# Kernel optimization log

Hardware: AMD Instinct MI355X
Metric: run time of the kernel (lower is better)

## Reference

```python
import jax, jax.numpy as jnp
import numpy as np
import math

B, LQ, LK = 4, 512, 512
D_MODEL, NHEAD, NLABELS = 512, 8, 8
D_Q = D_MODEL // NHEAD


def setup_inputs() -> dict:
    key = jax.random.key(0)
    ks = jax.random.split(key, 12)
    xavier = lambda k, shape: jax.random.uniform(
        k, shape, jnp.float32,
        -math.sqrt(6.0 / (shape[0] + shape[1])), math.sqrt(6.0 / (shape[0] + shape[1])))
    return {
        "q": jax.random.normal(ks[0], (B, LQ, D_MODEL), jnp.float32),
        "k": jax.random.normal(ks[1], (B, LK, D_MODEL), jnp.float32),
        "edge_mask": jax.random.randint(ks[2], (B, LQ, LK, NLABELS), 0, 2).astype(jnp.float32),
        "padding_mask": jax.random.randint(ks[3], (B, LQ, LK), 0, 2).astype(jnp.float32),
        "w_q_w": xavier(ks[4], (D_MODEL, D_MODEL)),
        "w_q_b": jnp.zeros((D_MODEL,), jnp.float32),
        "w_k": xavier(ks[5], (D_MODEL, D_MODEL)),
        "w_v": xavier(ks[6], (D_MODEL, D_MODEL)),
        "w_h_w": xavier(ks[7], (D_MODEL, D_MODEL)),
        "w_h_b": jnp.zeros((D_MODEL,), jnp.float32),
        "b_ks": xavier(ks[8], (NLABELS, D_Q)),
        "b_vs": xavier(ks[9], (NLABELS, D_Q)),
    }


def reference(q, k, edge_mask, padding_mask, w_q_w, w_q_b, w_k, w_v, w_h_w, w_h_b, b_ks, b_vs):
    sz_b, len_q, _ = q.shape
    len_k = k.shape[1]
    temp = np.power(D_Q, 0.5).astype(np.float32)

    # projections -> (nhead, B, L, d_q), matching torch permute(2,0,1,3)
    query = (q @ w_q_w.T + w_q_b).reshape(sz_b, len_q, NHEAD, D_Q).transpose(2, 0, 1, 3)
    key = (k @ w_k.T).reshape(sz_b, len_k, NHEAD, D_Q).transpose(2, 0, 1, 3)
    value = (k @ w_v.T).reshape(sz_b, len_k, NHEAD, D_Q).transpose(2, 0, 1, 3)

    # content scores + relation-bias scores
    qk = jnp.einsum('hbqd,hbkd->hbqk', query, key)
    key_rel = jnp.einsum('bqkl,ld->bqkd', edge_mask, b_ks)      # (B,Lq,Lk,d_q)
    qkr = jnp.einsum('hbqd,bqkd->hbqk', query, key_rel)
    output_attention_weights = (qk + qkr) / temp                # pre-mask, as returned by torch

    # mask where no edge label AND padding_mask==1
    relation_mask = (edge_mask.sum(-1) + (1.0 - padding_mask)) == 0  # (B,Lq,Lk)
    rm = relation_mask[None, :, :, :]                                # broadcast over heads
    attn = jnp.where(rm, -jnp.inf, output_attention_weights)
    attn = jax.nn.softmax(attn, axis=-1)
    attn = jnp.where(rm, 0.0, attn)

    # value aggregation: content + relation values
    qv = jnp.einsum('hbqk,hbkd->hbqd', attn, value)
    val_rel = jnp.einsum('bqkl,ld->bqkd', edge_mask, b_vs)
    qvr = jnp.einsum('hbqk,bqkd->hbqd', attn, val_rel)

    out = (qv + qvr).transpose(1, 2, 0, 3).reshape(sz_b, len_q, D_MODEL)
    out = out @ w_h_w.T + w_h_b
    return out, output_attention_weights.reshape(NHEAD * sz_b, len_q, len_k)
```

## Files before the change

kernel.cpp:

```cpp
#include <hip/hip_runtime.h>
#include <math.h>

#define NB 4
#define LQ 512
#define LK 512
#define DM 512
#define NH 8
#define DQ 64
#define NL 8

typedef short bf16x8 __attribute__((ext_vector_type(8)));
typedef float f32x4 __attribute__((ext_vector_type(4)));

__device__ __forceinline__ unsigned short f2bf(float x) {
    unsigned u = __float_as_uint(x);
    u += 0x7fff + ((u >> 16) & 1);
    return (unsigned short)(u >> 16);
}
__device__ __forceinline__ float bf2f(unsigned x) {
    return __uint_as_float(x << 16);
}

__device__ __forceinline__ void gld16(const void* g, void* l) {
    __builtin_amdgcn_global_load_lds(
        (const __attribute__((address_space(1))) void*)g,
        (__attribute__((address_space(3))) void*)l, 16, 0, 0);
}

template<int BM, int BN, int WR, int WC, int MI, int NI>
__device__ __forceinline__ void mfma_core(const unsigned short* __restrict__ Ag, int lda,
                                          const unsigned short* __restrict__ Bg, int ldb,
                                          int K, short* As, short* Bs,
                                          f32x4 (&acc)[MI][NI]) {
    const int tid = threadIdx.x;
    const int wave = tid >> 6, lane = tid & 63;
    const int quad = lane >> 4, l16 = lane & 15;
    const int wr = wave / WC, wc = wave % WC;
    constexpr int WMT = BM / WR, WNT = BN / WC;

    for (int k0 = 0; k0 < K; k0 += 32) {
        __syncthreads();
#pragma unroll
        for (int s = 0; s < BM / 64; ++s) {
            const int c = s * 256 + tid;
            gld16(Ag + (size_t)(c >> 2) * lda + k0 + (c & 3) * 8,
                  (char*)As + s * 4096 + wave * 1024);
        }
#pragma unroll
        for (int s = 0; s < BN / 64; ++s) {
            const int c = s * 256 + tid;
            gld16(Bg + (size_t)(c >> 2) * ldb + k0 + (c & 3) * 8,
                  (char*)Bs + s * 4096 + wave * 1024);
        }
        __syncthreads();

        bf16x8 af[MI], bf[NI];
#pragma unroll
        for (int i = 0; i < MI; ++i)
            af[i] = *(const bf16x8*)&As[(wr * WMT + i * 16 + l16) * 32 + quad * 8];
#pragma unroll
        for (int j = 0; j < NI; ++j)
            bf[j] = *(const bf16x8*)&Bs[(wc * WNT + j * 16 + l16) * 32 + quad * 8];
#pragma unroll
        for (int i = 0; i < MI; ++i)
#pragma unroll
            for (int j = 0; j < NI; ++j)
                acc[i][j] = __builtin_amdgcn_mfma_f32_16x16x32_bf16(af[i], bf[j], acc[i][j], 0, 0, 0);
    }
}

__global__ __launch_bounds__(256) void convert_kernel(
        const float* __restrict__ s0, const float* __restrict__ s1,
        const float* __restrict__ s2, const float* __restrict__ s3,
        const float* __restrict__ s4, const float* __restrict__ s5,
        unsigned short* __restrict__ d0, unsigned short* __restrict__ d1,
        unsigned short* __restrict__ d2, unsigned short* __restrict__ d3,
        unsigned short* __restrict__ d4, unsigned short* __restrict__ d5) {
    const float* s; unsigned short* d; int n;
    switch (blockIdx.y) {
        case 0: s = s0; d = d0; n = NB * LQ * DM; break;
        case 1: s = s1; d = d1; n = NB * LK * DM; break;
        case 2: s = s2; d = d2; n = DM * DM; break;
        case 3: s = s3; d = d3; n = DM * DM; break;
        case 4: s = s4; d = d4; n = DM * DM; break;
        default: s = s5; d = d5; n = DM * DM; break;
    }
    const int i = blockIdx.x * 256 + threadIdx.x;
    if (i * 8 >= n) return;
    const float4* sv = (const float4*)s;
    const float4 a = sv[2 * (size_t)i], b = sv[2 * (size_t)i + 1];
    uint4 o;
    o.x = (unsigned)f2bf(a.x) | ((unsigned)f2bf(a.y) << 16);
    o.y = (unsigned)f2bf(a.z) | ((unsigned)f2bf(a.w) << 16);
    o.z = (unsigned)f2bf(b.x) | ((unsigned)f2bf(b.y) << 16);
    o.w = (unsigned)f2bf(b.z) | ((unsigned)f2bf(b.w) << 16);
    *(uint4*)(d + (size_t)i * 8) = o;
}

__global__ __launch_bounds__(256) void proj_all(const unsigned short* __restrict__ qbf,
                                                const unsigned short* __restrict__ kbf,
                                                const unsigned short* __restrict__ wqb,
                                                const unsigned short* __restrict__ wkb,
                                                const unsigned short* __restrict__ wvb,
                                                const float* __restrict__ w_q_b,
                                                unsigned short* __restrict__ Qp,
                                                unsigned short* __restrict__ Kp,
                                                unsigned short* __restrict__ Vt) {
    __shared__ __align__(16) short As[64 * 32];
    __shared__ __align__(16) short Bs[64 * 32];
    const unsigned short* A; const unsigned short* W; const float* bias;
    unsigned short* C; int mode;
    switch (blockIdx.z) {
        case 0:  A = qbf; W = wqb; bias = w_q_b; C = Qp; mode = 0; break;
        case 1:  A = kbf; W = wkb; bias = nullptr; C = Kp; mode = 0; break;
        default: A = kbf; W = wvb; bias = nullptr; C = Vt; mode = 1; break;
    }
    f32x4 acc[2][2];
    const f32x4 zz = {0.f, 0.f, 0.f, 0.f};
#pragma unroll
    for (int i = 0; i < 2; ++i)
#pragma unroll
        for (int j = 0; j < 2; ++j) acc[i][j] = zz;
    const int m0 = blockIdx.x * 64, n0 = blockIdx.y * 64;
    mfma_core<64, 64, 2, 2, 2, 2>(A + (size_t)m0 * DM, DM, W + (size_t)n0 * DM, DM, DM, As, Bs, acc);
    const int tid = threadIdx.x, wave = tid >> 6, lane = tid & 63;
    const int quad = lane >> 4, l16 = lane & 15;
    const int wr = wave >> 1, wc = wave & 1;
#pragma unroll
    for (int i = 0; i < 2; ++i)
#pragma unroll
        for (int r = 0; r < 4; ++r) {
            const int gm = m0 + wr * 32 + i * 16 + quad * 4 + r;
#pragma unroll
            for (int j = 0; j < 2; ++j) {
                const int gn = n0 + wc * 32 + j * 16 + l16;
                float v = acc[i][j][r];
                if (bias) v += bias[gn];
                if (mode == 0) C[(size_t)gm * DM + gn] = f2bf(v);
                else C[(size_t)(gm >> 9) * (DM * LK) + (size_t)gn * LK + (gm & 511)] = f2bf(v);
            }
        }
}

__global__ __launch_bounds__(256) void qk_mfma(const unsigned short* __restrict__ Qp,
                                               const unsigned short* __restrict__ Kp,
                                               unsigned short* __restrict__ Sc) {
    __shared__ __align__(16) short As[64 * 32];
    __shared__ __align__(16) short Bs[64 * 32];
    f32x4 acc[2][2];
    const f32x4 zz = {0.f, 0.f, 0.f, 0.f};
#pragma unroll
    for (int i = 0; i < 2; ++i)
#pragma unroll
        for (int j = 0; j < 2; ++j) acc[i][j] = zz;
    const int z = blockIdx.z, h = z >> 2, b = z & 3;
    const int m0 = blockIdx.x * 64, n0 = blockIdx.y * 64;
    const unsigned short* Ag = Qp + (size_t)(b * LQ + m0) * DM + h * DQ;
    const unsigned short* Bg = Kp + (size_t)(b * LK + n0) * DM + h * DQ;
    mfma_core<64, 64, 2, 2, 2, 2>(Ag, DM, Bg, DM, DQ, As, Bs, acc);
    const int tid = threadIdx.x, wave = tid >> 6, lane = tid & 63;
    const int quad = lane >> 4, l16 = lane & 15;
    const int wr = wave >> 1, wc = wave & 1;
    unsigned short* Cz = Sc + (size_t)z * LQ * LK;
#pragma unroll
    for (int i = 0; i < 2; ++i)
#pragma unroll
        for (int r = 0; r < 4; ++r) {
            const int gm = m0 + wr * 32 + i * 16 + quad * 4 + r;
#pragma unroll
            for (int j = 0; j < 2; ++j) {
                const int gn = n0 + wc * 32 + j * 16 + l16;
                Cz[(size_t)gm * LK + gn] = f2bf(acc[i][j][r]);
            }
        }
}

__global__ __launch_bounds__(512) void softmax_kernel(const float* __restrict__ em,
                                                      const float* __restrict__ pad,
                                                      const unsigned short* __restrict__ Qp,
                                                      const float* __restrict__ b_ks,
                                                      const unsigned short* __restrict__ Sc,
                                                      float* __restrict__ weights,
                                                      unsigned short* __restrict__ attn,
                                                      float* __restrict__ Tb) {
    const int tid = threadIdx.x, wave = tid >> 6, lane = tid & 63;
    const int bq = blockIdx.x, b = bq >> 9, q = bq & 511;
    const int h = wave, z = h * NB + b;

    const float qd = bf2f(Qp[(size_t)bq * DM + h * DQ + lane]);
    float sv[NL];
#pragma unroll
    for (int l = 0; l < NL; ++l) {
        float p = qd * b_ks[l * DQ + lane];
#pragma unroll
        for (int o = 1; o < 64; o <<= 1) p += __shfl_xor(p, o, 64);
        sv[l] = p;
    }

    float4 ev[16];
    const float* eb = em + (size_t)bq * (LK * NL);
#pragma unroll
    for (int j = 0; j < 8; ++j) {
        const int k = lane + 64 * j;
        ev[2 * j]     = *(const float4*)(eb + k * 8);
        ev[2 * j + 1] = *(const float4*)(eb + k * 8 + 4);
    }
    float padv[8];
#pragma unroll
    for (int j = 0; j < 8; ++j) padv[j] = pad[(size_t)bq * LK + lane + 64 * j];
    const unsigned short* sp = Sc + ((size_t)z * LQ + q) * LK;
    float qk8[8];
#pragma unroll
    for (int j = 0; j < 8; ++j) qk8[j] = bf2f(sp[lane + 64 * j]);

    const size_t rowbase = ((size_t)z * LQ + q) * LK;
    float wv8[8], m8[8];
#pragma unroll
    for (int j = 0; j < 8; ++j) {
        const float4 a = ev[2 * j], c = ev[2 * j + 1];
        const float rel = a.x * sv[0] + a.y * sv[1] + a.z * sv[2] + a.w * sv[3]
                        + c.x * sv[4] + c.y * sv[5] + c.z * sv[6] + c.w * sv[7];
        const float es = ((a.x + a.y) + (a.z + a.w)) + ((c.x + c.y) + (c.z + c.w));
        const float wv = (qk8[j] + rel) * 0.125f;
        wv8[j] = wv;
        m8[j] = ((es + 1.0f - padv[j]) == 0.0f) ? -__builtin_inff() : wv;
        weights[rowbase + lane + 64 * j] = wv;
    }

    float mx = m8[0];
#pragma unroll
    for (int j = 1; j < 8; ++j) mx = fmaxf(mx, m8[j]);
#pragma unroll
    for (int o = 1; o < 64; o <<= 1) mx = fmaxf(mx, __shfl_xor(mx, o, 64));

    float e8[8], ss = 0.f;
#pragma unroll
    for (int j = 0; j < 8; ++j) { e8[j] = __expf(m8[j] - mx); ss += e8[j]; }
#pragma unroll
    for (int o = 1; o < 64; o <<= 1) ss += __shfl_xor(ss, o, 64);
    const float inv = 1.0f / ss;

    float tl[NL] = {0.f, 0.f, 0.f, 0.f, 0.f, 0.f, 0.f, 0.f};
#pragma unroll
    for (int j = 0; j < 8; ++j) {
        const float a_ = e8[j] * inv;
        attn[rowbase + lane + 64 * j] = f2bf(a_);
        const float4 a = ev[2 * j], c = ev[2 * j + 1];
        tl[0] = fmaf(a_, a.x, tl[0]); tl[1] = fmaf(a_, a.y, tl[1]);
        tl[2] = fmaf(a_, a.z, tl[2]); tl[3] = fmaf(a_, a.w, tl[3]);
        tl[4] = fmaf(a_, c.x, tl[4]); tl[5] = fmaf(a_, c.y, tl[5]);
        tl[6] = fmaf(a_, c.z, tl[6]); tl[7] = fmaf(a_, c.w, tl[7]);
    }
#pragma unroll
    for (int o = 1; o < 64; o <<= 1)
#pragma unroll
        for (int l = 0; l < NL; ++l) tl[l] += __shfl_xor(tl[l], o, 64);
    if (lane == 0) {
        float* tp = Tb + ((size_t)z * LQ + q) * NL;
#pragma unroll
        for (int l = 0; l < NL; ++l) tp[l] = tl[l];
    }
}

__global__ __launch_bounds__(256) void qv_mfma(const unsigned short* __restrict__ Attn,
                                               const unsigned short* __restrict__ Vt,
                                               const float* __restrict__ Tb,
                                               const float* __restrict__ b_vs,
                                               unsigned short* __restrict__ Hb) {
    __shared__ __align__(16) short As[64 * 32];
    __shared__ __align__(16) short Bs[64 * 32];
    f32x4 acc[2][2];
    const f32x4 zz = {0.f, 0.f, 0.f, 0.f};
#pragma unroll
    for (int i = 0; i < 2; ++i)
#pragma unroll
        for (int j = 0; j < 2; ++j) acc[i][j] = zz;
    const int z = blockIdx.z, h = z >> 2, b = z & 3;
    const int m0 = blockIdx.x * 64;
    const unsigned short* Ag = Attn + (size_t)z * LQ * LK + (size_t)m0 * LK;
    const unsigned short* Bg = Vt + (size_t)b * (DM * LK) + (size_t)(h * DQ) * LK;
    mfma_core<64, 64, 2, 2, 2, 2>(Ag, LK, Bg, LK, LK, As, Bs, acc);
    const int tid = threadIdx.x, wave = tid >> 6, lane = tid & 63;
    const int quad = lane >> 4, l16 = lane & 15;
    const int wr = wave >> 1, wc = wave & 1;
    float bvv[2][NL];
#pragma unroll
    for (int j = 0; j < 2; ++j)
#pragma unroll
        for (int l = 0; l < NL; ++l) bvv[j][l] = b_vs[l * DQ + wc * 32 + j * 16 + l16];
#pragma unroll
    for (int i = 0; i < 2; ++i)
#pragma unroll
        for (int r = 0; r < 4; ++r) {
            const int qrow = m0 + wr * 32 + i * 16 + quad * 4 + r;
            const float* t8 = Tb + ((size_t)z * LQ + qrow) * NL;
            float t[NL];
#pragma unroll
            for (int l = 0; l < NL; ++l) t[l] = t8[l];
#pragma unroll
            for (int j = 0; j < 2; ++j) {
                const int d = wc * 32 + j * 16 + l16;
                float qvr = 0.f;
#pragma unroll
                for (int l = 0; l < NL; ++l) qvr = fmaf(t[l], bvv[j][l], qvr);
                Hb[(size_t)(b * LQ + qrow) * DM + h * DQ + d] = f2bf(acc[i][j][r] + qvr);
            }
        }
}

__global__ __launch_bounds__(256) void outproj_mfma(const unsigned short* __restrict__ A,
                                                    const unsigned short* __restrict__ W,
                                                    const float* __restrict__ bias,
                                                    float* __restrict__ C) {
    __shared__ __align__(16) short As[64 * 32];
    __shared__ __align__(16) short Bs[64 * 32];
    f32x4 acc[2][2];
    const f32x4 zz = {0.f, 0.f, 0.f, 0.f};
#pragma unroll
    for (int i = 0; i < 2; ++i)
#pragma unroll
        for (int j = 0; j < 2; ++j) acc[i][j] = zz;
    const int m0 = blockIdx.x * 64, n0 = blockIdx.y * 64;
    mfma_core<64, 64, 2, 2, 2, 2>(A + (size_t)m0 * DM, DM, W + (size_t)n0 * DM, DM, DM, As, Bs, acc);
    const int tid = threadIdx.x, wave = tid >> 6, lane = tid & 63;
    const int quad = lane >> 4, l16 = lane & 15;
    const int wr = wave >> 1, wc = wave & 1;
#pragma unroll
    for (int i = 0; i < 2; ++i)
#pragma unroll
        for (int r = 0; r < 4; ++r) {
            const int gm = m0 + wr * 32 + i * 16 + quad * 4 + r;
#pragma unroll
            for (int j = 0; j < 2; ++j) {
                const int gn = n0 + wc * 32 + j * 16 + l16;
                C[(size_t)gm * DM + gn] = acc[i][j][r] + bias[gn];
            }
        }
}

extern "C" void kernel_launch(void* const* d_in, const int* in_sizes, int n_in,
                              void* d_out, int out_size, void* d_ws, size_t ws_size,
                              hipStream_t stream) {
    const float* q     = (const float*)d_in[0];
    const float* k     = (const float*)d_in[1];
    const float* em    = (const float*)d_in[2];
    const float* pad   = (const float*)d_in[3];
    const float* w_q_w = (const float*)d_in[4];
    const float* w_q_b = (const float*)d_in[5];
    const float* w_k   = (const float*)d_in[6];
    const float* w_v   = (const float*)d_in[7];
    const float* w_h_w = (const float*)d_in[8];
    const float* w_h_b = (const float*)d_in[9];
    const float* b_ks  = (const float*)d_in[10];
    const float* b_vs  = (const float*)d_in[11];

    float* out     = (float*)d_out;
    float* weights = out + (size_t)NB * LQ * DM;

    char* ws = (char*)d_ws;
    unsigned short* qbf = (unsigned short*)(ws + 0);
    unsigned short* kbf = (unsigned short*)(ws + 2097152);
    unsigned short* wqb = (unsigned short*)(ws + 4194304);
    unsigned short* wkb = (unsigned short*)(ws + 4718592);
    unsigned short* wvb = (unsigned short*)(ws + 5242880);
    unsigned short* whb = (unsigned short*)(ws + 5767168);
    unsigned short* Qp  = (unsigned short*)(ws + 6291456);
    unsigned short* Kp  = (unsigned short*)(ws + 8388608);
    unsigned short* Vt  = (unsigned short*)(ws + 10485760);
    unsigned short* Hb  = (unsigned short*)(ws + 12582912);
    unsigned short* Att = (unsigned short*)(ws + 14680064);
    unsigned short* Sc  = (unsigned short*)(ws + 31457280);
    float*          Tb  = (float*)(ws + 48234496);

    convert_kernel<<<dim3(512, 6), 256, 0, stream>>>(q, k, w_q_w, w_k, w_v, w_h_w,
                                                     qbf, kbf, wqb, wkb, wvb, whb);
    proj_all<<<dim3(32, 8, 3), 256, 0, stream>>>(qbf, kbf, wqb, wkb, wvb, w_q_b, Qp, Kp, Vt);
    qk_mfma<<<dim3(8, 8, 32), 256, 0, stream>>>(Qp, Kp, Sc);
    softmax_kernel<<<dim3(NB * LQ), dim3(512), 0, stream>>>(em, pad, Qp, b_ks, Sc,
                                                            weights, Att, Tb);
    qv_mfma<<<dim3(8, 1, 32), 256, 0, stream>>>(Att, Vt, Tb, b_vs, Hb);
    outproj_mfma<<<dim3(32, 8), 256, 0, stream>>>(Hb, whb, w_h_b, out);
}
```

Measured before the change: 173.3 us.

## Fuse fp32-to-bf16 conversion into GEMMs and retile qk and qv kernels

Drops the separate conversion kernel. The projection and output GEMMs now load fp32 inputs and weights directly and pack them to bf16 in registers before the LDS store. qk_mfma moves to 128x128 tiles with the whole K=64 staged at once, and qv_mfma uses 512 threads with 8 waves splitting the 64x64 tile. This saves a launch and a round trip through global memory. The cost is fp32 loads that are twice as wide and synchronous register staging in place of direct global-to-LDS loads.

```diff
diff --git a/kernel.cpp b/kernel.cpp
--- a/kernel.cpp
+++ b/kernel.cpp
@@ -20,112 +20,75 @@
 __device__ __forceinline__ float bf2f(unsigned x) {
     return __uint_as_float(x << 16);
 }
-
-__device__ __forceinline__ void gld16(const void* g, void* l) {
-    __builtin_amdgcn_global_load_lds(
-        (const __attribute__((address_space(1))) void*)g,
-        (__attribute__((address_space(3))) void*)l, 16, 0, 0);
-}
-
-template<int BM, int BN, int WR, int WC, int MI, int NI>
-__device__ __forceinline__ void mfma_core(const unsigned short* __restrict__ Ag, int lda,
-                                          const unsigned short* __restrict__ Bg, int ldb,
-                                          int K, short* As, short* Bs,
-                                          f32x4 (&acc)[MI][NI]) {
-    const int tid = threadIdx.x;
-    const int wave = tid >> 6, lane = tid & 63;
-    const int quad = lane >> 4, l16 = lane & 15;
-    const int wr = wave / WC, wc = wave % WC;
-    constexpr int WMT = BM / WR, WNT = BN / WC;
-
-    for (int k0 = 0; k0 < K; k0 += 32) {
-        __syncthreads();
-#pragma unroll
-        for (int s = 0; s < BM / 64; ++s) {
-            const int c = s * 256 + tid;
-            gld16(Ag + (size_t)(c >> 2) * lda + k0 + (c & 3) * 8,
-                  (char*)As + s * 4096 + wave * 1024);
-        }
-#pragma unroll
-        for (int s = 0; s < BN / 64; ++s) {
-            const int c = s * 256 + tid;
-            gld16(Bg + (size_t)(c >> 2) * ldb + k0 + (c & 3) * 8,
-                  (char*)Bs + s * 4096 + wave * 1024);
-        }
-        __syncthreads();
-
-        bf16x8 af[MI], bf[NI];
-#pragma unroll
-        for (int i = 0; i < MI; ++i)
-            af[i] = *(const bf16x8*)&As[(wr * WMT + i * 16 + l16) * 32 + quad * 8];
-#pragma unroll
-        for (int j = 0; j < NI; ++j)
-            bf[j] = *(const bf16x8*)&Bs[(wc * WNT + j * 16 + l16) * 32 + quad * 8];
-#pragma unroll
-        for (int i = 0; i < MI; ++i)
-#pragma unroll
-            for (int j = 0; j < NI; ++j)
-                acc[i][j] = __builtin_amdgcn_mfma_f32_16x16x32_bf16(af[i], bf[j], acc[i][j], 0, 0, 0);
-    }
-}
-
-__global__ __launch_bounds__(256) void convert_kernel(
-        const float* __restrict__ s0, const float* __restrict__ s1,
-        const float* __restrict__ s2, const float* __restrict__ s3,
-        const float* __restrict__ s4, const float* __restrict__ s5,
-        unsigned short* __restrict__ d0, unsigned short* __restrict__ d1,
-        unsigned short* __restrict__ d2, unsigned short* __restrict__ d3,
-        unsigned short* __restrict__ d4, unsigned short* __restrict__ d5) {
-    const float* s; unsigned short* d; int n;
-    switch (blockIdx.y) {
-        case 0: s = s0; d = d0; n = NB * LQ * DM; break;
-        case 1: s = s1; d = d1; n = NB * LK * DM; break;
-        case 2: s = s2; d = d2; n = DM * DM; break;
-        case 3: s = s3; d = d3; n = DM * DM; break;
-        case 4: s = s4; d = d4; n = DM * DM; break;
-        default: s = s5; d = d5; n = DM * DM; break;
-    }
-    const int i = blockIdx.x * 256 + threadIdx.x;
-    if (i * 8 >= n) return;
-    const float4* sv = (const float4*)s;
-    const float4 a = sv[2 * (size_t)i], b = sv[2 * (size_t)i + 1];
+__device__ __forceinline__ uint4 pack8(float4 a, float4 b) {
     uint4 o;
     o.x = (unsigned)f2bf(a.x) | ((unsigned)f2bf(a.y) << 16);
     o.y = (unsigned)f2bf(a.z) | ((unsigned)f2bf(a.w) << 16);
     o.z = (unsigned)f2bf(b.x) | ((unsigned)f2bf(b.y) << 16);
     o.w = (unsigned)f2bf(b.z) | ((unsigned)f2bf(b.w) << 16);
-    *(uint4*)(d + (size_t)i * 8) = o;
-}
-
-__global__ __launch_bounds__(256) void proj_all(const unsigned short* __restrict__ qbf,
-                                                const unsigned short* __restrict__ kbf,
-                                                const unsigned short* __restrict__ wqb,
-                                                const unsigned short* __restrict__ wkb,
-                                                const unsigned short* __restrict__ wvb,
+    return o;
+}
+
+__device__ __forceinline__ void gld16(const void* g, void* l) {
+    __builtin_amdgcn_global_load_lds(
+        (const __attribute__((address_space(1))) void*)g,
+        (__attribute__((address_space(3))) void*)l, 16, 0, 0);
+}
+
+__global__ __launch_bounds__(256) void proj_all(const float* __restrict__ qg,
+                                                const float* __restrict__ kg,
+                                                const float* __restrict__ wq,
+                                                const float* __restrict__ wk,
+                                                const float* __restrict__ wv,
                                                 const float* __restrict__ w_q_b,
                                                 unsigned short* __restrict__ Qp,
                                                 unsigned short* __restrict__ Kp,
                                                 unsigned short* __restrict__ Vt) {
     __shared__ __align__(16) short As[64 * 32];
     __shared__ __align__(16) short Bs[64 * 32];
-    const unsigned short* A; const unsigned short* W; const float* bias;
-    unsigned short* C; int mode;
+    const float* A; const float* W; const float* bias; unsigned short* C; int mode;
     switch (blockIdx.z) {
-        case 0:  A = qbf; W = wqb; bias = w_q_b; C = Qp; mode = 0; break;
-        case 1:  A = kbf; W = wkb; bias = nullptr; C = Kp; mode = 0; break;
-        default: A = kbf; W = wvb; bias = nullptr; C = Vt; mode = 1; break;
-    }
+        case 0:  A = qg; W = wq; bias = w_q_b;  C = Qp; mode = 0; break;
+        case 1:  A = kg; W = wk; bias = nullptr; C = Kp; mode = 0; break;
+        default: A = kg; W = wv; bias = nullptr; C = Vt; mode = 1; break;
+    }
+    const int tid = threadIdx.x, wave = tid >> 6, lane = tid & 63;
+    const int quad = lane >> 4, l16 = lane & 15;
+    const int wr = wave >> 1, wc = wave & 1;
+    const int m0 = blockIdx.x * 64, n0 = blockIdx.y * 64;
+    const int srow = tid >> 2, scol = (tid & 3) * 8;
+    const float* Ab = A + (size_t)(m0 + srow) * DM + scol;
+    const float* Wb = W + (size_t)(n0 + srow) * DM + scol;
+
     f32x4 acc[2][2];
     const f32x4 zz = {0.f, 0.f, 0.f, 0.f};
 #pragma unroll
     for (int i = 0; i < 2; ++i)
 #pragma unroll
         for (int j = 0; j < 2; ++j) acc[i][j] = zz;
-    const int m0 = blockIdx.x * 64, n0 = blockIdx.y * 64;
-    mfma_core<64, 64, 2, 2, 2, 2>(A + (size_t)m0 * DM, DM, W + (size_t)n0 * DM, DM, DM, As, Bs, acc);
-    const int tid = threadIdx.x, wave = tid >> 6, lane = tid & 63;
-    const int quad = lane >> 4, l16 = lane & 15;
-    const int wr = wave >> 1, wc = wave & 1;
+
+    for (int k0 = 0; k0 < DM; k0 += 32) {
+        const float4 a0 = *(const float4*)(Ab + k0);
+        const float4 a1 = *(const float4*)(Ab + k0 + 4);
+        const float4 b0 = *(const float4*)(Wb + k0);
+        const float4 b1 = *(const float4*)(Wb + k0 + 4);
+        __syncthreads();
+        *(uint4*)&As[srow * 32 + scol] = pack8(a0, a1);
+        *(uint4*)&Bs[srow * 32 + scol] = pack8(b0, b1);
+        __syncthreads();
+        bf16x8 af[2], bf[2];
+#pragma unroll
+        for (int i = 0; i < 2; ++i)
+            af[i] = *(const bf16x8*)&As[(wr * 32 + i * 16 + l16) * 32 + quad * 8];
+#pragma unroll
+        for (int j = 0; j < 2; ++j)
+            bf[j] = *(const bf16x8*)&Bs[(wc * 32 + j * 16 + l16) * 32 + quad * 8];
+#pragma unroll
+        for (int i = 0; i < 2; ++i)
+#pragma unroll
+            for (int j = 0; j < 2; ++j)
+                acc[i][j] = __builtin_amdgcn_mfma_f32_16x16x32_bf16(af[i], bf[j], acc[i][j], 0, 0, 0);
+    }
 #pragma unroll
     for (int i = 0; i < 2; ++i)
 #pragma unroll
@@ -145,31 +108,58 @@
 __global__ __launch_bounds__(256) void qk_mfma(const unsigned short* __restrict__ Qp,
                                                const unsigned short* __restrict__ Kp,
                                                unsigned short* __restrict__ Sc) {
-    __shared__ __align__(16) short As[64 * 32];
-    __shared__ __align__(16) short Bs[64 * 32];
-    f32x4 acc[2][2];
-    const f32x4 zz = {0.f, 0.f, 0.f, 0.f};
-#pragma unroll
-    for (int i = 0; i < 2; ++i)
-#pragma unroll
-        for (int j = 0; j < 2; ++j) acc[i][j] = zz;
+    __shared__ __align__(16) short As[2][128 * 32];
+    __shared__ __align__(16) short Bs[2][128 * 32];
+    const int tid = threadIdx.x, wave = tid >> 6, lane = tid & 63;
+    const int quad = lane >> 4, l16 = lane & 15;
+    const int wr = wave >> 1, wc = wave & 1;
     const int z = blockIdx.z, h = z >> 2, b = z & 3;
-    const int m0 = blockIdx.x * 64, n0 = blockIdx.y * 64;
+    const int m0 = blockIdx.x * 128, n0 = blockIdx.y * 128;
     const unsigned short* Ag = Qp + (size_t)(b * LQ + m0) * DM + h * DQ;
     const unsigned short* Bg = Kp + (size_t)(b * LK + n0) * DM + h * DQ;
-    mfma_core<64, 64, 2, 2, 2, 2>(Ag, DM, Bg, DM, DQ, As, Bs, acc);
-    const int tid = threadIdx.x, wave = tid >> 6, lane = tid & 63;
-    const int quad = lane >> 4, l16 = lane & 15;
-    const int wr = wave >> 1, wc = wave & 1;
+
+#pragma unroll
+    for (int s = 0; s < 2; ++s)
+#pragma unroll
+        for (int it = 0; it < 2; ++it) {
+            const int c = it * 256 + tid;
+            gld16(Ag + (size_t)(c >> 2) * DM + s * 32 + (c & 3) * 8,
+                  (char*)As[s] + it * 4096 + wave * 1024);
+            gld16(Bg + (size_t)(c >> 2) * DM + s * 32 + (c & 3) * 8,
+                  (char*)Bs[s] + it * 4096 + wave * 1024);
+        }
+    __syncthreads();
+
+    f32x4 acc[4][4];
+    const f32x4 zz = {0.f, 0.f, 0.f, 0.f};
+#pragma unroll
+    for (int i = 0; i < 4; ++i)
+#pragma unroll
+        for (int j = 0; j < 4; ++j) acc[i][j] = zz;
+#pragma unroll
+    for (int s = 0; s < 2; ++s) {
+        bf16x8 af[4], bf[4];
+#pragma unroll
+        for (int i = 0; i < 4; ++i)
+            af[i] = *(const bf16x8*)&As[s][(wr * 64 + i * 16 + l16) * 32 + quad * 8];
+#pragma unroll
+        for (int j = 0; j < 4; ++j)
+            bf[j] = *(const bf16x8*)&Bs[s][(wc * 64 + j * 16 + l16) * 32 + quad * 8];
+#pragma unroll
+        for (int i = 0; i < 4; ++i)
+#pragma unroll
+            for (int j = 0; j < 4; ++j)
+                acc[i][j] = __builtin_amdgcn_mfma_f32_16x16x32_bf16(af[i], bf[j], acc[i][j], 0, 0, 0);
+    }
     unsigned short* Cz = Sc + (size_t)z * LQ * LK;
 #pragma unroll
-    for (int i = 0; i < 2; ++i)
+    for (int i = 0; i < 4; ++i)
 #pragma unroll
         for (int r = 0; r < 4; ++r) {
-            const int gm = m0 + wr * 32 + i * 16 + quad * 4 + r;
-#pragma unroll
-            for (int j = 0; j < 2; ++j) {
-                const int gn = n0 + wc * 32 + j * 16 + l16;
+            const int gm = m0 + wr * 64 + i * 16 + quad * 4 + r;
+#pragma unroll
+            for (int j = 0; j < 4; ++j) {
+                const int gn = n0 + wc * 64 + j * 16 + l16;
                 Cz[(size_t)gm * LK + gn] = f2bf(acc[i][j][r]);
             }
         }
@@ -262,69 +252,103 @@
     }
 }
 
-__global__ __launch_bounds__(256) void qv_mfma(const unsigned short* __restrict__ Attn,
+__global__ __launch_bounds__(512) void qv_mfma(const unsigned short* __restrict__ Attn,
                                                const unsigned short* __restrict__ Vt,
                                                const float* __restrict__ Tb,
                                                const float* __restrict__ b_vs,
                                                unsigned short* __restrict__ Hb) {
     __shared__ __align__(16) short As[64 * 32];
     __shared__ __align__(16) short Bs[64 * 32];
-    f32x4 acc[2][2];
-    const f32x4 zz = {0.f, 0.f, 0.f, 0.f};
-#pragma unroll
-    for (int i = 0; i < 2; ++i)
-#pragma unroll
-        for (int j = 0; j < 2; ++j) acc[i][j] = zz;
+    const int tid = threadIdx.x, wave = tid >> 6, lane = tid & 63;
+    const int quad = lane >> 4, l16 = lane & 15;
+    const int wr = wave >> 2, wc = wave & 3;
     const int z = blockIdx.z, h = z >> 2, b = z & 3;
     const int m0 = blockIdx.x * 64;
     const unsigned short* Ag = Attn + (size_t)z * LQ * LK + (size_t)m0 * LK;
     const unsigned short* Bg = Vt + (size_t)b * (DM * LK) + (size_t)(h * DQ) * LK;
-    mfma_core<64, 64, 2, 2, 2, 2>(Ag, LK, Bg, LK, LK, As, Bs, acc);
-    const int tid = threadIdx.x, wave = tid >> 6, lane = tid & 63;
-    const int quad = lane >> 4, l16 = lane & 15;
-    const int wr = wave >> 1, wc = wave & 1;
-    float bvv[2][NL];
-#pragma unroll
-    for (int j = 0; j < 2; ++j)
-#pragma unroll
-        for (int l = 0; l < NL; ++l) bvv[j][l] = b_vs[l * DQ + wc * 32 + j * 16 + l16];
+
+    f32x4 acc[2];
+    const f32x4 zz = {0.f, 0.f, 0.f, 0.f};
+    acc[0] = zz; acc[1] = zz;
+    const int c = tid & 255;
+
+    for (int k0 = 0; k0 < LK; k0 += 32) {
+        __syncthreads();
+        if (tid < 256)
+            gld16(Ag + (size_t)(c >> 2) * LK + k0 + (c & 3) * 8,
+                  (char*)As + wave * 1024);
+        else
+            gld16(Bg + (size_t)(c >> 2) * LK + k0 + (c & 3) * 8,
+                  (char*)Bs + (wave - 4) * 1024);
+        __syncthreads();
+        bf16x8 af[2], bf;
+#pragma unroll
+        for (int i = 0; i < 2; ++i)
+            af[i] = *(const bf16x8*)&As[(wr * 32 + i * 16 + l16) * 32 + quad * 8];
+        bf = *(const bf16x8*)&Bs[(wc * 16 + l16) * 32 + quad * 8];
+#pragma unroll
+        for (int i = 0; i < 2; ++i)
+            acc[i] = __builtin_amdgcn_mfma_f32_16x16x32_bf16(af[i], bf, acc[i], 0, 0, 0);
+    }
+    const int d = wc * 16 + l16;
+    float bvv[NL];
+#pragma unroll
+    for (int l = 0; l < NL; ++l) bvv[l] = b_vs[l * DQ + d];
 #pragma unroll
     for (int i = 0; i < 2; ++i)
 #pragma unroll
         for (int r = 0; r < 4; ++r) {
             const int qrow = m0 + wr * 32 + i * 16 + quad * 4 + r;
             const float* t8 = Tb + ((size_t)z * LQ + qrow) * NL;
-            float t[NL];
-#pragma unroll
-            for (int l = 0; l < NL; ++l) t[l] = t8[l];
-#pragma unroll
-            for (int j = 0; j < 2; ++j) {
-                const int d = wc * 32 + j * 16 + l16;
-                float qvr = 0.f;
-#pragma unroll
-                for (int l = 0; l < NL; ++l) qvr = fmaf(t[l], bvv[j][l], qvr);
-                Hb[(size_t)(b * LQ + qrow) * DM + h * DQ + d] = f2bf(acc[i][j][r] + qvr);
-            }
-        }
-}
-
-__global__ __launch_bounds__(256) void outproj_mfma(const unsigned short* __restrict__ A,
-                                                    const unsigned short* __restrict__ W,
+            float qvr = 0.f;
+#pragma unroll
+            for (int l = 0; l < NL; ++l) qvr = fmaf(t8[l], bvv[l], qvr);
+            Hb[(size_t)(b * LQ + qrow) * DM + h * DQ + d] = f2bf(acc[i][r] + qvr);
+        }
+}
+
+__global__ __launch_bounds__(256) void outproj_mfma(const unsigned short* __restrict__ Hb,
+                                                    const float* __restrict__ W,
                                                     const float* __restrict__ bias,
                                                     float* __restrict__ C) {
     __shared__ __align__(16) short As[64 * 32];
     __shared__ __align__(16) short Bs[64 * 32];
+    const int tid = threadIdx.x, wave = tid >> 6, lane = tid & 63;
+    const int quad = lane >> 4, l16 = lane & 15;
+    const int wr = wave >> 1, wc = wave & 1;
+    const int m0 = blockIdx.x * 64, n0 = blockIdx.y * 64;
+    const int srow = tid >> 2, scol = (tid & 3) * 8;
+    const unsigned short* Ag = Hb + (size_t)m0 * DM;
+    const float* Wb = W + (size_t)(n0 + srow) * DM + scol;
+
     f32x4 acc[2][2];
     const f32x4 zz = {0.f, 0.f, 0.f, 0.f};
 #pragma unroll
     for (int i = 0; i < 2; ++i)
 #pragma unroll
         for (int j = 0; j < 2; ++j) acc[i][j] = zz;
-    const int m0 = blockIdx.x * 64, n0 = blockIdx.y * 64;
-    mfma_core<64, 64, 2, 2, 2, 2>(A + (size_t)m0 * DM, DM, W + (size_t)n0 * DM, DM, DM, As, Bs, acc);
-    const int tid = threadIdx.x, wave = tid >> 6, lane = tid & 63;
-    const int quad = lane >> 4, l16 = lane & 15;
-    const int wr = wave >> 1, wc = wave & 1;
+
+    for (int k0 = 0; k0 < DM; k0 += 32) {
+        const float4 b0 = *(const float4*)(Wb + k0);
+        const float4 b1 = *(const float4*)(Wb + k0 + 4);
+        __syncthreads();
+        gld16(Ag + (size_t)(tid >> 2) * DM + k0 + (tid & 3) * 8,
+              (char*)As + wave * 1024);
+        *(uint4*)&Bs[srow * 32 + scol] = pack8(b0, b1);
+        __syncthreads();
+        bf16x8 af[2], bf[2];
+#pragma unroll
+        for (int i = 0; i < 2; ++i)
+            af[i] = *(const bf16x8*)&As[(wr * 32 + i * 16 + l16) * 32 + quad * 8];
+#pragma unroll
+        for (int j = 0; j < 2; ++j)
+            bf[j] = *(const bf16x8*)&Bs[(wc * 32 + j * 16 + l16) * 32 + quad * 8];
+#pragma unroll
+        for (int i = 0; i < 2; ++i)
+#pragma unroll
+            for (int j = 0; j < 2; ++j)
+                acc[i][j] = __builtin_amdgcn_mfma_f32_16x16x32_bf16(af[i], bf[j], acc[i][j], 0, 0, 0);
+    }
 #pragma unroll
     for (int i = 0; i < 2; ++i)
 #pragma unroll
@@ -358,26 +382,18 @@
     float* weights = out + (size_t)NB * LQ * DM;
 
     char* ws = (char*)d_ws;
-    unsigned short* qbf = (unsigned short*)(ws + 0);
-    unsigned short* kbf = (unsigned short*)(ws + 2097152);
-    unsigned short* wqb = (unsigned short*)(ws + 4194304);
-    unsigned short* wkb = (unsigned short*)(ws + 4718592);
-    unsigned short* wvb = (unsigned short*)(ws + 5242880);
-    unsigned short* whb = (unsigned short*)(ws + 5767168);
-    unsigned short* Qp  = (unsigned short*)(ws + 6291456);
-    unsigned short* Kp  = (unsigned short*)(ws + 8388608);
-    unsigned short* Vt  = (unsigned short*)(ws + 10485760);
-    unsigned short* Hb  = (unsigned short*)(ws + 12582912);
-    unsigned short* Att = (unsigned short*)(ws + 14680064);
-    unsigned short* Sc  = (unsigned short*)(ws + 31457280);
-    float*          Tb  = (float*)(ws + 48234496);
-
-    convert_kernel<<<dim3(512, 6), 256, 0, stream>>>(q, k, w_q_w, w_k, w_v, w_h_w,
-                                                     qbf, kbf, wqb, wkb, wvb, whb);
-    proj_all<<<dim3(32, 8, 3), 256, 0, stream>>>(qbf, kbf, wqb, wkb, wvb, w_q_b, Qp, Kp, Vt);
-    qk_mfma<<<dim3(8, 8, 32), 256, 0, stream>>>(Qp, Kp, Sc);
+    unsigned short* Qp  = (unsigned short*)(ws + 0);
+    unsigned short* Kp  = (unsigned short*)(ws + 2097152);
+    unsigned short* Vt  = (unsigned short*)(ws + 4194304);
+    unsigned short* Hb  = (unsigned short*)(ws + 6291456);
+    unsigned short* Att = (unsigned short*)(ws + 8388608);
+    unsigned short* Sc  = (unsigned short*)(ws + 25165824);
+    float*          Tb  = (float*)(ws + 41943040);
+
+    proj_all<<<dim3(32, 8, 3), 256, 0, stream>>>(q, k, w_q_w, w_k, w_v, w_q_b, Qp, Kp, Vt);
+    qk_mfma<<<dim3(4, 4, 32), 256, 0, stream>>>(Qp, Kp, Sc);
     softmax_kernel<<<dim3(NB * LQ), dim3(512), 0, stream>>>(em, pad, Qp, b_ks, Sc,
                                                             weights, Att, Tb);
-    qv_mfma<<<dim3(8, 1, 32), 256, 0, stream>>>(Att, Vt, Tb, b_vs, Hb);
-    outproj_mfma<<<dim3(32, 8), 256, 0, stream>>>(Hb, whb, w_h_b, out);
-}
+    qv_mfma<<<dim3(8, 1, 32), 512, 0, stream>>>(Att, Vt, Tb, b_vs, Hb);
+    outproj_mfma<<<dim3(32, 8), 256, 0, stream>>>(Hb, w_h_w, w_h_b, out);
+}
```

After: 183.1 us. 1.06x slower.
